# Performance work log

Measured on AMD Instinct MI355X. Metric: run time of the kernel, lower is better.

## Reference

```python
import jax, jax.numpy as jnp
import numpy as np

B, C, H, W = 16, 256, 56, 56
G, K, R = 16, 3, 2
CR = C // R          # reduced channels = 128
KKG = K * K * G      # span output channels = 144
EPS = 1e-5


def setup_inputs() -> dict:
    key = jax.random.key(0)
    ks = jax.random.split(key, 5)
    return {
        "x": jax.random.normal(ks[0], (B, C, H, W), jnp.float32),
        "w_reduce": jax.random.normal(ks[1], (CR, C), jnp.float32) * 0.05,
        "b_reduce": jax.random.normal(ks[2], (CR,), jnp.float32) * 0.05,
        "gamma": jnp.ones((CR,), jnp.float32),
        "beta": jnp.zeros((CR,), jnp.float32),
        "w_span": jax.random.normal(ks[3], (KKG, CR), jnp.float32) * 0.05,
        "b_span": jax.random.normal(ks[4], (KKG,), jnp.float32) * 0.05,
    }


def _conv1x1(x, w, bias):
    # 1x1 conv == channel contraction
    return jnp.einsum('bchw,oc->bohw', x, w) + bias[None, :, None, None]


def _involution(x, w_reduce, b_reduce, gamma, beta, w_span, b_span):
    b, c, h, w = x.shape
    # kernel-generation branch: reduce -> BN (batch stats) -> ReLU -> span
    t = _conv1x1(x, w_reduce, b_reduce)
    mu = t.mean(axis=(0, 2, 3), keepdims=True)
    var = t.var(axis=(0, 2, 3), keepdims=True)  # biased, as torch BN training
    t = (t - mu) * jax.lax.rsqrt(var + EPS)
    t = t * gamma[None, :, None, None] + beta[None, :, None, None]
    t = jax.nn.relu(t)
    kern = _conv1x1(t, w_span, b_span)  # [b, k*k*g, h, w]
    # 'b (k j g) h w -> b g (k j) h w'
    kern = kern.reshape(b, K, K, G, h, w).transpose(0, 3, 1, 2, 4, 5)
    kern = kern.reshape(b, G, K * K, h, w)
    # unfold x into [b, g, d, k*k, h, w] via shifted padded slices (no dense im2col buffer write pattern beyond necessity)
    p = K // 2
    xp = jnp.pad(x, ((0, 0), (0, 0), (p, p), (p, p)))
    patches = jnp.stack(
        [xp[:, :, i:i + h, j:j + w] for i in range(K) for j in range(K)],
        axis=2)  # [b, c, k*k, h, w]
    patches = patches.reshape(b, G, c // G, K * K, h, w)
    out = jnp.einsum('bgdxhw,bgxhw->bgdhw', patches, kern)  # weighted window sum
    return out.reshape(b, c, h, w)


def reference(x, w_reduce, b_reduce, gamma, beta, w_span, b_span):
    return _involution(x, w_reduce, b_reduce, gamma, beta, w_span, b_span)
```

## Files before the change

### kernel.cpp

```cpp
#include <hip/hip_runtime.h>

#define B_   16
#define C_   256
#define HW_  3136
#define W_   56
#define CR_  128
#define KKG_ 144
#define G_   16
#define NPOS (B_*HW_)
#define EPS_ 1e-5f
#define NBLK 784

typedef float f32x4 __attribute__((ext_vector_type(4)));
typedef short s16x8 __attribute__((ext_vector_type(8)));
typedef short s16x4 __attribute__((ext_vector_type(4)));

#define T2_OFF_B    0
#define KERN_OFF_B  12845056
#define GP_OFF_B    27295744
#define STAT_OFF_B  28098560
#define WBFR_OFF_B  28099584
#define WBFS_OFF_B  28165120

__device__ inline unsigned short f2bf(float f) {
    unsigned u = __float_as_uint(f);
    u += 0x7fff + ((u >> 16) & 1);
    return (unsigned short)(u >> 16);
}
__device__ inline float bf2f(unsigned short h) {
    return __uint_as_float(((unsigned)h) << 16);
}

__global__ __launch_bounds__(256) void prep_cast(
    const float* __restrict__ w_reduce, const float* __restrict__ w_span,
    unsigned short* __restrict__ wbfr, unsigned short* __restrict__ wbfs)
{
    int idx = blockIdx.x * 256 + threadIdx.x;
    if (idx < 32768) {
        wbfr[idx] = f2bf(w_reduce[idx]);
    } else {
        int k = idx - 32768;
        if (k < 18432) wbfs[k] = f2bf(w_span[k]);
    }
}

__global__ __launch_bounds__(256) void reduce_mfma(
    const float* __restrict__ x, const unsigned short* __restrict__ wbfr,
    unsigned short* __restrict__ t2, float* __restrict__ gp)
{
    __shared__ __align__(16) short as_[128 * 40];
    __shared__ __align__(16) short bs_[64 * 40];
    __shared__ float redp[128][2], redq[128][2];

    const int tid = threadIdx.x;
    const int lane = tid & 63, wv = tid >> 6;
    const int q = lane >> 4, i = lane & 15;
    const int mrow = (wv >> 1) * 64, nrow = (wv & 1) * 32;
    const int blk = blockIdx.x;
    const int b = blk / 49;
    const int p0 = (blk % 49) * 64;

    const float* xb = x + (size_t)b * C_ * HW_ + p0;

    const int o_a = tid >> 1, half = tid & 1;
    const int cp = tid >> 4, rq = tid & 15;

    f32x4 acc[4][2] = {};

    for (int c0 = 0; c0 < C_; c0 += 32) {
        {
            const unsigned short* src = wbfr + o_a * C_ + c0 + half * 16;
            s16x8 w0 = *(const s16x8*)src;
            s16x8 w1 = *(const s16x8*)(src + 8);
            *(s16x8*)&as_[o_a * 40 + half * 16] = w0;
            *(s16x8*)&as_[o_a * 40 + half * 16 + 8] = w1;
        }
        {
            const float* s0 = xb + (size_t)(c0 + 2 * cp) * HW_ + rq * 4;
            float4 va = *(const float4*)s0;
            float4 vb = *(const float4*)(s0 + HW_);
            float a4[4] = {va.x, va.y, va.z, va.w};
            float b4[4] = {vb.x, vb.y, vb.z, vb.w};
            #pragma unroll
            for (int j = 0; j < 4; j++) {
                unsigned pk = (unsigned)f2bf(a4[j]) | ((unsigned)f2bf(b4[j]) << 16);
                *(unsigned*)&bs_[(rq * 4 + j) * 40 + 2 * cp] = pk;
            }
        }
        __syncthreads();
        s16x8 af[4], bfr[2];
        #pragma unroll
        for (int mt = 0; mt < 4; mt++)
            af[mt] = *(const s16x8*)&as_[(mrow + mt * 16 + i) * 40 + q * 8];
        #pragma unroll
        for (int nt = 0; nt < 2; nt++)
            bfr[nt] = *(const s16x8*)&bs_[(nrow + nt * 16 + i) * 40 + q * 8];
        #pragma unroll
        for (int mt = 0; mt < 4; mt++)
            #pragma unroll
            for (int nt = 0; nt < 2; nt++)
                acc[mt][nt] = __builtin_amdgcn_mfma_f32_16x16x32_bf16(
                    af[mt], bfr[nt], acc[mt][nt], 0, 0, 0);
        __syncthreads();
    }

    #pragma unroll
    for (int mt = 0; mt < 4; mt++) {
        #pragma unroll
        for (int nt = 0; nt < 2; nt++) {
            #pragma unroll
            for (int reg = 0; reg < 4; reg++) {
                int o = mrow + mt * 16 + q * 4 + reg;
                int p = p0 + nrow + nt * 16 + i;
                t2[((size_t)o * B_ + b) * HW_ + p] = f2bf(acc[mt][nt][reg]);
            }
        }
        #pragma unroll
        for (int reg = 0; reg < 4; reg++) {
            float v0 = acc[mt][0][reg], v1 = acc[mt][1][reg];
            float s = v0 + v1;
            float ss = v0 * v0 + v1 * v1;
            #pragma unroll
            for (int m = 1; m < 16; m <<= 1) {
                s  += __shfl_xor(s, m);
                ss += __shfl_xor(ss, m);
            }
            if (i == 0) {
                int o = mrow + mt * 16 + q * 4 + reg;
                redp[o][wv & 1] = s;
                redq[o][wv & 1] = ss;
            }
        }
    }
    __syncthreads();
    if (tid < 128)
        gp[(size_t)blk * 256 + tid] = redp[tid][0] + redp[tid][1];
    else
        gp[(size_t)blk * 256 + tid] = redq[tid - 128][0] + redq[tid - 128][1];
}

__global__ __launch_bounds__(256) void bn_finalize(
    const float* __restrict__ gp, const float* __restrict__ gamma,
    const float* __restrict__ beta, float* __restrict__ stats)
{
    const int o = blockIdx.x;
    const int tid = threadIdx.x;
    float s = 0.f, ss = 0.f;
    for (int blk = tid; blk < NBLK; blk += 256) {
        s  += gp[(size_t)blk * 256 + o];
        ss += gp[(size_t)blk * 256 + 128 + o];
    }
    #pragma unroll
    for (int m = 1; m < 64; m <<= 1) {
        s  += __shfl_xor(s, m);
        ss += __shfl_xor(ss, m);
    }
    __shared__ float rs[4], rss[4];
    if ((tid & 63) == 0) { rs[tid >> 6] = s; rss[tid >> 6] = ss; }
    __syncthreads();
    if (tid == 0) {
        s  = rs[0] + rs[1] + rs[2] + rs[3];
        ss = rss[0] + rss[1] + rss[2] + rss[3];
        float inv_n = 1.0f / (float)NPOS;
        float mu = s * inv_n;
        float var = ss * inv_n - mu * mu;
        float sc = gamma[o] * rsqrtf(var + EPS_);
        stats[o] = sc;
        stats[128 + o] = beta[o] - mu * sc;
    }
}

__global__ __launch_bounds__(256) void span_mfma(
    const unsigned short* __restrict__ t2, const unsigned short* __restrict__ wbfs,
    const float* __restrict__ b_span, const float* __restrict__ stats,
    unsigned short* __restrict__ kern)
{
    __shared__ __align__(16) short as_[144 * 40];
    __shared__ __align__(16) short bs_[64 * 40];
    __shared__ float scs[128], shs[128], bsp[144];

    const int tid = threadIdx.x;
    const int lane = tid & 63, wv = tid >> 6;
    const int q = lane >> 4, i = lane & 15;
    const int blk = blockIdx.x;
    const int b = blk / 49;
    const int p0 = (blk % 49) * 64;

    if (tid < 128) { scs[tid] = stats[tid]; shs[tid] = stats[128 + tid]; }
    if (tid < 144) bsp[tid] = b_span[tid];
    __syncthreads();

    const int op = tid >> 4, seg = tid & 15;

    f32x4 acc[9] = {};

    for (int c0 = 0; c0 < CR_; c0 += 32) {
        #pragma unroll
        for (int P = 0; P < 3; P++) {
            int idx = P * 256 + tid;
            if (idx < 576) {
                int row = idx >> 2, k8 = idx & 3;
                *(s16x8*)&as_[row * 40 + k8 * 8] =
                    *(const s16x8*)&wbfs[row * CR_ + c0 + k8 * 8];
            }
        }
        {
            int cA = c0 + 2 * op;
            const unsigned short* tA = t2 + ((size_t)cA * B_ + b) * HW_ + p0 + seg * 4;
            s16x4 vA = *(const s16x4*)tA;
            s16x4 vB = *(const s16x4*)(tA + (size_t)B_ * HW_);
            float sA = scs[cA], hA = shs[cA];
            float sB = scs[cA + 1], hB = shs[cA + 1];
            #pragma unroll
            for (int j = 0; j < 4; j++) {
                float fa = fmaxf(fmaf(bf2f((unsigned short)vA[j]), sA, hA), 0.0f);
                float fb = fmaxf(fmaf(bf2f((unsigned short)vB[j]), sB, hB), 0.0f);
                unsigned pk = (unsigned)f2bf(fa) | ((unsigned)f2bf(fb) << 16);
                *(unsigned*)&bs_[(seg * 4 + j) * 40 + 2 * op] = pk;
            }
        }
        __syncthreads();
        s16x8 bfrag = *(const s16x8*)&bs_[(wv * 16 + i) * 40 + q * 8];
        #pragma unroll
        for (int mt = 0; mt < 9; mt++) {
            s16x8 af = *(const s16x8*)&as_[(mt * 16 + i) * 40 + q * 8];
            acc[mt] = __builtin_amdgcn_mfma_f32_16x16x32_bf16(af, bfrag, acc[mt], 0, 0, 0);
        }
        __syncthreads();
    }

    const int p = p0 + wv * 16 + i;
    #pragma unroll
    for (int mt = 0; mt < 9; mt++) {
        #pragma unroll
        for (int reg = 0; reg < 4; reg++) {
            int o2 = mt * 16 + q * 4 + reg;
            kern[((size_t)b * KKG_ + o2) * HW_ + p] = f2bf(acc[mt][reg] + bsp[o2]);
        }
    }
}

__global__ __launch_bounds__(256) void involution_apply(
    const float* __restrict__ x, const unsigned short* __restrict__ kern,
    float* __restrict__ out)
{
    int gtid = blockIdx.x * 256 + threadIdx.x;
    int pix = gtid % HW_;
    int bg  = gtid / HW_;
    int g = bg & 15;
    int b = bg >> 4;
    int h = pix / W_;
    int w = pix % W_;

    const unsigned short* kb = kern + (size_t)b * KKG_ * HW_ + pix;
    float kv[9];
    #pragma unroll
    for (int kk = 0; kk < 9; kk++)
        kv[kk] = bf2f(kb[(size_t)(kk * G_ + g) * HW_]);

    float acc[16];
    #pragma unroll
    for (int d = 0; d < 16; d++) acc[d] = 0.0f;

    const float* xb = x + (size_t)(b * C_ + g * 16) * HW_;
    #pragma unroll
    for (int di = 0; di < 3; di++) {
        int hh = h + di - 1;
        if (hh < 0 || hh >= W_) continue;
        #pragma unroll
        for (int dj = 0; dj < 3; dj++) {
            int ww = w + dj - 1;
            if (ww < 0 || ww >= W_) continue;
            float kval = kv[di * 3 + dj];
            int off = hh * W_ + ww;
            #pragma unroll
            for (int d = 0; d < 16; d++)
                acc[d] = fmaf(xb[(size_t)d * HW_ + off], kval, acc[d]);
        }
    }
    float* ob = out + (size_t)(b * C_ + g * 16) * HW_ + pix;
    #pragma unroll
    for (int d = 0; d < 16; d++) ob[(size_t)d * HW_] = acc[d];
}

extern "C" void kernel_launch(void* const* d_in, const int* in_sizes, int n_in,
                              void* d_out, int out_size, void* d_ws, size_t ws_size,
                              hipStream_t stream) {
    const float* x        = (const float*)d_in[0];
    const float* w_reduce = (const float*)d_in[1];
    const float* gamma    = (const float*)d_in[3];
    const float* beta     = (const float*)d_in[4];
    const float* w_span   = (const float*)d_in[5];
    const float* b_span   = (const float*)d_in[6];
    float* out = (float*)d_out;

    char* wsb = (char*)d_ws;
    unsigned short* t2   = (unsigned short*)(wsb + T2_OFF_B);
    unsigned short* kern = (unsigned short*)(wsb + KERN_OFF_B);
    float*          gp    = (float*)(wsb + GP_OFF_B);
    float*          stats = (float*)(wsb + STAT_OFF_B);
    unsigned short* wbfr = (unsigned short*)(wsb + WBFR_OFF_B);
    unsigned short* wbfs = (unsigned short*)(wsb + WBFS_OFF_B);

    prep_cast<<<200, 256, 0, stream>>>(w_reduce, w_span, wbfr, wbfs);
    reduce_mfma<<<NBLK, 256, 0, stream>>>(x, wbfr, t2, gp);
    bn_finalize<<<128, 256, 0, stream>>>(gp, gamma, beta, stats);
    span_mfma<<<NBLK, 256, 0, stream>>>(t2, wbfs, b_span, stats, kern);
    involution_apply<<<(B_ * G_ * HW_) / 256, 256, 0, stream>>>(x, kern, out);
}
```

Measured before the change: 160.5 us.

## Double-buffer GEMM LDS tiles, read weights from global, vectorize involution over 4 pixels

```diff
diff --git a/kernel.cpp b/kernel.cpp
--- a/kernel.cpp
+++ b/kernel.cpp
@@ -48,8 +48,7 @@
     const float* __restrict__ x, const unsigned short* __restrict__ wbfr,
     unsigned short* __restrict__ t2, float* __restrict__ gp)
 {
-    __shared__ __align__(16) short as_[128 * 40];
-    __shared__ __align__(16) short bs_[64 * 40];
+    __shared__ __align__(16) short bs_[2][64 * 40];
     __shared__ float redp[128][2], redq[128][2];
 
     const int tid = threadIdx.x;
@@ -61,47 +60,56 @@
     const int p0 = (blk % 49) * 64;
 
     const float* xb = x + (size_t)b * C_ * HW_ + p0;
-
-    const int o_a = tid >> 1, half = tid & 1;
     const int cp = tid >> 4, rq = tid & 15;
 
     f32x4 acc[4][2] = {};
 
-    for (int c0 = 0; c0 < C_; c0 += 32) {
-        {
-            const unsigned short* src = wbfr + o_a * C_ + c0 + half * 16;
-            s16x8 w0 = *(const s16x8*)src;
-            s16x8 w1 = *(const s16x8*)(src + 8);
-            *(s16x8*)&as_[o_a * 40 + half * 16] = w0;
-            *(s16x8*)&as_[o_a * 40 + half * 16 + 8] = w1;
-        }
-        {
-            const float* s0 = xb + (size_t)(c0 + 2 * cp) * HW_ + rq * 4;
-            float4 va = *(const float4*)s0;
-            float4 vb = *(const float4*)(s0 + HW_);
-            float a4[4] = {va.x, va.y, va.z, va.w};
-            float b4[4] = {vb.x, vb.y, vb.z, vb.w};
-            #pragma unroll
-            for (int j = 0; j < 4; j++) {
-                unsigned pk = (unsigned)f2bf(a4[j]) | ((unsigned)f2bf(b4[j]) << 16);
-                *(unsigned*)&bs_[(rq * 4 + j) * 40 + 2 * cp] = pk;
-            }
-        }
+    {
+        const float* s0 = xb + (size_t)(2 * cp) * HW_ + rq * 4;
+        float4 va = *(const float4*)s0;
+        float4 vb = *(const float4*)(s0 + HW_);
+        float a4[4] = {va.x, va.y, va.z, va.w};
+        float b4[4] = {vb.x, vb.y, vb.z, vb.w};
+        #pragma unroll
+        for (int j = 0; j < 4; j++) {
+            unsigned pk = (unsigned)f2bf(a4[j]) | ((unsigned)f2bf(b4[j]) << 16);
+            *(unsigned*)&bs_[0][(rq * 4 + j) * 40 + 2 * cp] = pk;
+        }
+    }
+
+    #pragma unroll
+    for (int k = 0; k < 8; k++) {
+        const int buf = k & 1;
+        float4 va_n, vb_n;
+        if (k < 7) {
+            const float* s0 = xb + (size_t)((k + 1) * 32 + 2 * cp) * HW_ + rq * 4;
+            va_n = *(const float4*)s0;
+            vb_n = *(const float4*)(s0 + HW_);
+        }
+        s16x8 af[4];
+        #pragma unroll
+        for (int mt = 0; mt < 4; mt++)
+            af[mt] = *(const s16x8*)&wbfr[(size_t)(mrow + mt * 16 + i) * C_ + k * 32 + q * 8];
         __syncthreads();
-        s16x8 af[4], bfr[2];
-        #pragma unroll
-        for (int mt = 0; mt < 4; mt++)
-            af[mt] = *(const s16x8*)&as_[(mrow + mt * 16 + i) * 40 + q * 8];
+        s16x8 bfr[2];
         #pragma unroll
         for (int nt = 0; nt < 2; nt++)
-            bfr[nt] = *(const s16x8*)&bs_[(nrow + nt * 16 + i) * 40 + q * 8];
+            bfr[nt] = *(const s16x8*)&bs_[buf][(nrow + nt * 16 + i) * 40 + q * 8];
         #pragma unroll
         for (int mt = 0; mt < 4; mt++)
             #pragma unroll
             for (int nt = 0; nt < 2; nt++)
                 acc[mt][nt] = __builtin_amdgcn_mfma_f32_16x16x32_bf16(
                     af[mt], bfr[nt], acc[mt][nt], 0, 0, 0);
-        __syncthreads();
+        if (k < 7) {
+            float a4[4] = {va_n.x, va_n.y, va_n.z, va_n.w};
+            float b4[4] = {vb_n.x, vb_n.y, vb_n.z, vb_n.w};
+            #pragma unroll
+            for (int j = 0; j < 4; j++) {
+                unsigned pk = (unsigned)f2bf(a4[j]) | ((unsigned)f2bf(b4[j]) << 16);
+                *(unsigned*)&bs_[buf ^ 1][(rq * 4 + j) * 40 + 2 * cp] = pk;
+            }
+        }
     }
 
     #pragma unroll
@@ -175,8 +183,7 @@
     const float* __restrict__ b_span, const float* __restrict__ stats,
     unsigned short* __restrict__ kern)
 {
-    __shared__ __align__(16) short as_[144 * 40];
-    __shared__ __align__(16) short bs_[64 * 40];
+    __shared__ __align__(16) short bs_[2][64 * 40];
     __shared__ float scs[128], shs[128], bsp[144];
 
     const int tid = threadIdx.x;
@@ -194,39 +201,53 @@
 
     f32x4 acc[9] = {};
 
-    for (int c0 = 0; c0 < CR_; c0 += 32) {
-        #pragma unroll
-        for (int P = 0; P < 3; P++) {
-            int idx = P * 256 + tid;
-            if (idx < 576) {
-                int row = idx >> 2, k8 = idx & 3;
-                *(s16x8*)&as_[row * 40 + k8 * 8] =
-                    *(const s16x8*)&wbfs[row * CR_ + c0 + k8 * 8];
-            }
-        }
-        {
-            int cA = c0 + 2 * op;
-            const unsigned short* tA = t2 + ((size_t)cA * B_ + b) * HW_ + p0 + seg * 4;
-            s16x4 vA = *(const s16x4*)tA;
-            s16x4 vB = *(const s16x4*)(tA + (size_t)B_ * HW_);
-            float sA = scs[cA], hA = shs[cA];
-            float sB = scs[cA + 1], hB = shs[cA + 1];
+    {
+        int cA = 2 * op;
+        const unsigned short* tA = t2 + ((size_t)cA * B_ + b) * HW_ + p0 + seg * 4;
+        s16x4 vA = *(const s16x4*)tA;
+        s16x4 vB = *(const s16x4*)(tA + (size_t)B_ * HW_);
+        float sA = scs[cA], hA = shs[cA];
+        float sB = scs[cA + 1], hB = shs[cA + 1];
+        #pragma unroll
+        for (int j = 0; j < 4; j++) {
+            float fa = fmaxf(fmaf(bf2f((unsigned short)vA[j]), sA, hA), 0.0f);
+            float fb = fmaxf(fmaf(bf2f((unsigned short)vB[j]), sB, hB), 0.0f);
+            unsigned pk = (unsigned)f2bf(fa) | ((unsigned)f2bf(fb) << 16);
+            *(unsigned*)&bs_[0][(seg * 4 + j) * 40 + 2 * op] = pk;
+        }
+    }
+
+    #pragma unroll
+    for (int k = 0; k < 4; k++) {
+        const int buf = k & 1;
+        s16x4 vA_n, vB_n;
+        int cA_n = 0;
+        if (k < 3) {
+            cA_n = (k + 1) * 32 + 2 * op;
+            const unsigned short* tA = t2 + ((size_t)cA_n * B_ + b) * HW_ + p0 + seg * 4;
+            vA_n = *(const s16x4*)tA;
+            vB_n = *(const s16x4*)(tA + (size_t)B_ * HW_);
+        }
+        s16x8 af[9];
+        #pragma unroll
+        for (int mt = 0; mt < 9; mt++)
+            af[mt] = *(const s16x8*)&wbfs[(size_t)(mt * 16 + i) * CR_ + k * 32 + q * 8];
+        __syncthreads();
+        s16x8 bfrag = *(const s16x8*)&bs_[buf][(wv * 16 + i) * 40 + q * 8];
+        #pragma unroll
+        for (int mt = 0; mt < 9; mt++)
+            acc[mt] = __builtin_amdgcn_mfma_f32_16x16x32_bf16(af[mt], bfrag, acc[mt], 0, 0, 0);
+        if (k < 3) {
+            float sA = scs[cA_n], hA = shs[cA_n];
+            float sB = scs[cA_n + 1], hB = shs[cA_n + 1];
             #pragma unroll
             for (int j = 0; j < 4; j++) {
-                float fa = fmaxf(fmaf(bf2f((unsigned short)vA[j]), sA, hA), 0.0f);
-                float fb = fmaxf(fmaf(bf2f((unsigned short)vB[j]), sB, hB), 0.0f);
+                float fa = fmaxf(fmaf(bf2f((unsigned short)vA_n[j]), sA, hA), 0.0f);
+                float fb = fmaxf(fmaf(bf2f((unsigned short)vB_n[j]), sB, hB), 0.0f);
                 unsigned pk = (unsigned)f2bf(fa) | ((unsigned)f2bf(fb) << 16);
-                *(unsigned*)&bs_[(seg * 4 + j) * 40 + 2 * op] = pk;
-            }
-        }
-        __syncthreads();
-        s16x8 bfrag = *(const s16x8*)&bs_[(wv * 16 + i) * 40 + q * 8];
-        #pragma unroll
-        for (int mt = 0; mt < 9; mt++) {
-            s16x8 af = *(const s16x8*)&as_[(mt * 16 + i) * 40 + q * 8];
-            acc[mt] = __builtin_amdgcn_mfma_f32_16x16x32_bf16(af, bfrag, acc[mt], 0, 0, 0);
-        }
-        __syncthreads();
+                *(unsigned*)&bs_[buf ^ 1][(seg * 4 + j) * 40 + 2 * op] = pk;
+            }
+        }
     }
 
     const int p = p0 + wv * 16 + i;
@@ -245,42 +266,51 @@
     float* __restrict__ out)
 {
     int gtid = blockIdx.x * 256 + threadIdx.x;
-    int pix = gtid % HW_;
-    int bg  = gtid / HW_;
+    int pix4 = gtid % 784;
+    int bg   = gtid / 784;
     int g = bg & 15;
     int b = bg >> 4;
-    int h = pix / W_;
-    int w = pix % W_;
+    int h  = pix4 / 14;
+    int w0 = (pix4 % 14) * 4;
+    int pix = h * W_ + w0;
 
     const unsigned short* kb = kern + (size_t)b * KKG_ * HW_ + pix;
-    float kv[9];
-    #pragma unroll
-    for (int kk = 0; kk < 9; kk++)
-        kv[kk] = bf2f(kb[(size_t)(kk * G_ + g) * HW_]);
-
-    float acc[16];
-    #pragma unroll
-    for (int d = 0; d < 16; d++) acc[d] = 0.0f;
-
+    float kv[9][4];
+    #pragma unroll
+    for (int kk = 0; kk < 9; kk++) {
+        s16x4 kvv = *(const s16x4*)&kb[(size_t)(kk * G_ + g) * HW_];
+        #pragma unroll
+        for (int j = 0; j < 4; j++) kv[kk][j] = bf2f((unsigned short)kvv[j]);
+    }
+
+    const bool wl = (w0 > 0), wr = (w0 < W_ - 4);
     const float* xb = x + (size_t)(b * C_ + g * 16) * HW_;
-    #pragma unroll
-    for (int di = 0; di < 3; di++) {
-        int hh = h + di - 1;
-        if (hh < 0 || hh >= W_) continue;
-        #pragma unroll
-        for (int dj = 0; dj < 3; dj++) {
-            int ww = w + dj - 1;
-            if (ww < 0 || ww >= W_) continue;
-            float kval = kv[di * 3 + dj];
-            int off = hh * W_ + ww;
-            #pragma unroll
-            for (int d = 0; d < 16; d++)
-                acc[d] = fmaf(xb[(size_t)d * HW_ + off], kval, acc[d]);
-        }
-    }
     float* ob = out + (size_t)(b * C_ + g * 16) * HW_ + pix;
-    #pragma unroll
-    for (int d = 0; d < 16; d++) ob[(size_t)d * HW_] = acc[d];
+
+    #pragma unroll 4
+    for (int d = 0; d < 16; d++) {
+        const float* xd = xb + (size_t)d * HW_;
+        float a0 = 0.f, a1 = 0.f, a2 = 0.f, a3 = 0.f;
+        #pragma unroll
+        for (int di = 0; di < 3; di++) {
+            int hh = h + di - 1;
+            if (hh < 0 || hh >= W_) continue;
+            const float* rowp = xd + hh * W_ + w0;
+            float4 m = *(const float4*)rowp;
+            float e0 = wl ? rowp[-1] : 0.f;
+            float e5 = wr ? rowp[4]  : 0.f;
+            float e[6] = {e0, m.x, m.y, m.z, m.w, e5};
+            #pragma unroll
+            for (int dj = 0; dj < 3; dj++) {
+                const float* kvt = kv[di * 3 + dj];
+                a0 = fmaf(e[0 + dj], kvt[0], a0);
+                a1 = fmaf(e[1 + dj], kvt[1], a1);
+                a2 = fmaf(e[2 + dj], kvt[2], a2);
+                a3 = fmaf(e[3 + dj], kvt[3], a3);
+            }
+        }
+        *(float4*)(ob + (size_t)d * HW_) = make_float4(a0, a1, a2, a3);
+    }
 }
 
 extern "C" void kernel_launch(void* const* d_in, const int* in_sizes, int n_in,
@@ -306,5 +336,5 @@
     reduce_mfma<<<NBLK, 256, 0, stream>>>(x, wbfr, t2, gp);
     bn_finalize<<<128, 256, 0, stream>>>(gp, gamma, beta, stats);
     span_mfma<<<NBLK, 256, 0, stream>>>(t2, wbfs, b_span, stats, kern);
-    involution_apply<<<(B_ * G_ * HW_) / 256, 256, 0, stream>>>(x, kern, out);
-}
+    involution_apply<<<NBLK, 256, 0, stream>>>(x, kern, out);
+}
```

Measured after the change: 182.2 us. +13.5%, slower.
